# Kernel tuning notes

Measured on AMD Instinct MI355X. Metric: run time of the kernel, lower is better.

## Reference

```python
import jax, jax.numpy as jnp
import numpy as np

D_MODEL = 2048
N_HEAD = 16
HEAD_DIM = D_MODEL // N_HEAD
FF_MULT = 4
LN_EPS = 1e-5


def layer_norm(x, w, b):
    mu = jnp.mean(x, axis=-1, keepdims=True)
    var = jnp.mean(jnp.square(x - mu), axis=-1, keepdims=True)
    return (x - mu) * jax.lax.rsqrt(var + LN_EPS) * w + b


def setup_inputs() -> dict:
    key = jax.random.key(0)
    ks = jax.random.split(key, 10)
    B, S, D = 2, 2048, D_MODEL
    s = 1.0 / np.sqrt(D)
    inp = {
        "x": jax.random.normal(ks[0], (B, S, D), jnp.float32),
        "token_emb": jax.random.normal(ks[1], (B, S, D), jnp.float32),
        # torch Linear weights are (out_features, in_features)
        "Wq": jax.random.normal(ks[2], (D, D), jnp.float32) * s,
        "Wk": jax.random.normal(ks[3], (D, D), jnp.float32) * s,
        "Wv": jax.random.normal(ks[4], (D, D), jnp.float32) * s,
        "Wo": jax.random.normal(ks[5], (D, D), jnp.float32) * s,
        "W1": jax.random.normal(ks[6], (FF_MULT * D, D), jnp.float32) * s,
        "W2": jax.random.normal(ks[7], (D, FF_MULT * D), jnp.float32) * (1.0 / np.sqrt(FF_MULT * D)),
        "ln1_w": jnp.ones((D,), jnp.float32),
        "ln1_b": jnp.zeros((D,), jnp.float32),
        "ln2_w": jnp.ones((D,), jnp.float32),
        "ln2_b": jnp.zeros((D,), jnp.float32),
    }
    return inp


def reference(x, token_emb, Wq, Wk, Wv, Wo, W1, W2, ln1_w, ln1_b, ln2_w, ln2_b):
    B, S, D = x.shape
    H, Hd = N_HEAD, HEAD_DIM

    h_norm = layer_norm(x, ln1_w, ln1_b)
    # torch Linear: y = x @ W.T
    q = (h_norm @ Wq.T).reshape(B, S, H, Hd).transpose(0, 2, 1, 3)  # (B,H,S,Hd)
    k = (h_norm @ Wk.T).reshape(B, S, H, Hd).transpose(0, 2, 1, 3)
    v = (token_emb @ Wv.T).reshape(B, S, H, Hd).transpose(0, 2, 1, 3)

    scores = jnp.einsum("bhqd,bhkd->bhqk", q, k) / np.sqrt(Hd)
    causal = jnp.tril(jnp.ones((S, S), bool))  # (S,S)
    scores = jnp.where(causal, scores, -jnp.inf)
    weights = jax.nn.softmax(scores, axis=-1)

    attn = jnp.einsum("bhqk,bhkd->bhqd", weights, v)
    attn = attn.transpose(0, 2, 1, 3).reshape(B, S, D)
    attn = attn @ Wo.T
    x = x + attn

    h_ffn = layer_norm(x, ln2_w, ln2_b)
    ffn = jax.nn.gelu(h_ffn @ W1.T, approximate=False) @ W2.T
    return x + ffn
```

## Files before the change

kernel.cpp:

```cpp
#include <hip/hip_runtime.h>
#include <hip/hip_bf16.h>
#include <math.h>

#define D_MODEL 2048
#define SEQ     2048
#define BATCH   2
#define NTOK    (BATCH*SEQ)
#define NHEAD   16
#define HDIM    128
#define FF      8192

typedef float  f32x4  __attribute__((ext_vector_type(4)));
typedef __bf16 bf16x8 __attribute__((ext_vector_type(8)));

__device__ __forceinline__ unsigned short f2bfbits(float f) {
    unsigned u = __builtin_bit_cast(unsigned, f);
    return (unsigned short)((u + 0x7fffu + ((u >> 16) & 1u)) >> 16);
}
__device__ __forceinline__ __bf16 f2bf(float f) {
    unsigned short h = f2bfbits(f);
    return __builtin_bit_cast(__bf16, h);
}

__device__ __forceinline__ void gld_lds16(const void* g, void* l) {
    __builtin_amdgcn_global_load_lds(
        (const __attribute__((address_space(1))) unsigned int*)g,
        (__attribute__((address_space(3))) unsigned int*)l, 16, 0, 0);
}

__global__ __launch_bounds__(256) void cvt_all(
        const float* __restrict__ tok, const float* __restrict__ wq,
        const float* __restrict__ wk,  const float* __restrict__ wv,
        const float* __restrict__ wo,  const float* __restrict__ w1,
        const float* __restrict__ w2,
        __bf16* __restrict__ tokb, __bf16* __restrict__ wqb,
        __bf16* __restrict__ wkb,  __bf16* __restrict__ wvb,
        __bf16* __restrict__ wob,  __bf16* __restrict__ w1b,
        __bf16* __restrict__ w2b) {
    const size_t M4 = 4u * 1024 * 1024;
    size_t i = (size_t)blockIdx.x * 1024 + (size_t)threadIdx.x * 4;
    const float* src; __bf16* dst; size_t off;
    if      (i < 2*M4)  { src = tok; dst = tokb; off = i; }
    else if (i < 3*M4)  { src = wq;  dst = wqb;  off = i - 2*M4; }
    else if (i < 4*M4)  { src = wk;  dst = wkb;  off = i - 3*M4; }
    else if (i < 5*M4)  { src = wv;  dst = wvb;  off = i - 4*M4; }
    else if (i < 6*M4)  { src = wo;  dst = wob;  off = i - 5*M4; }
    else if (i < 10*M4) { src = w1;  dst = w1b;  off = i - 6*M4; }
    else                { src = w2;  dst = w2b;  off = i - 10*M4; }
    float4 v = *(const float4*)(src + off);
    ushort4 o;
    o.x = f2bfbits(v.x); o.y = f2bfbits(v.y);
    o.z = f2bfbits(v.z); o.w = f2bfbits(v.w);
    *(ushort4*)((unsigned short*)dst + off) = o;
}

__global__ __launch_bounds__(256) void add_reduce(
        const float* __restrict__ p0, const float* __restrict__ p1,
        const float* __restrict__ resid, float* __restrict__ out) {
    int i = blockIdx.x * 256 + threadIdx.x;
    float4 a = ((const float4*)p0)[i];
    float4 b = ((const float4*)p1)[i];
    float4 r = ((const float4*)resid)[i];
    float4 o;
    o.x = a.x + b.x + r.x; o.y = a.y + b.y + r.y;
    o.z = a.z + b.z + r.z; o.w = a.w + b.w + r.w;
    ((float4*)out)[i] = o;
}

__global__ __launch_bounds__(256) void ln_bf16(
        const float* __restrict__ x, const float* __restrict__ w,
        const float* __restrict__ b, __bf16* __restrict__ out) {
    const int row = blockIdx.x;
    const int tid = threadIdx.x;
    const float* xr = x + (size_t)row * D_MODEL;
    float4 v0 = *(const float4*)(xr + tid * 8);
    float4 v1 = *(const float4*)(xr + tid * 8 + 4);
    float va[8] = {v0.x, v0.y, v0.z, v0.w, v1.x, v1.y, v1.z, v1.w};
    float s = 0.f, ss = 0.f;
#pragma unroll
    for (int j = 0; j < 8; ++j) { s += va[j]; ss += va[j] * va[j]; }
#pragma unroll
    for (int m = 32; m; m >>= 1) { s += __shfl_xor(s, m, 64); ss += __shfl_xor(ss, m, 64); }
    __shared__ float red[8];
    const int wid = tid >> 6;
    if ((tid & 63) == 0) { red[wid * 2] = s; red[wid * 2 + 1] = ss; }
    __syncthreads();
    s  = red[0] + red[2] + red[4] + red[6];
    ss = red[1] + red[3] + red[5] + red[7];
    const float mu   = s * (1.0f / D_MODEL);
    const float var  = ss * (1.0f / D_MODEL) - mu * mu;
    const float rstd = rsqrtf(var + 1e-5f);
    const int c = tid * 8;
    ushort4 o0, o1;
    unsigned short ob[8];
#pragma unroll
    for (int j = 0; j < 8; ++j)
        ob[j] = f2bfbits((va[j] - mu) * rstd * w[c + j] + b[c + j]);
    o0.x = ob[0]; o0.y = ob[1]; o0.z = ob[2]; o0.w = ob[3];
    o1.x = ob[4]; o1.y = ob[5]; o1.z = ob[6]; o1.w = ob[7];
    ushort4* op = (ushort4*)(out + (size_t)row * D_MODEL + c);
    op[0] = o0; op[1] = o1;
}


template <int EPI, int MM>
__device__ __forceinline__ void gemm_epi(
        f32x4 (*acc)[4], int BMsz, int WMsz,
        int bm, int bn, int wm, int wn, int lhi, int l16,
        int M, int N, int slice,
        __bf16* __restrict__ Cb, float* __restrict__ Cf,
        const float* __restrict__ resid) {
#pragma unroll
    for (int m = 0; m < MM; ++m) {
        const int row = bm * BMsz + wm * WMsz + m * 16 + lhi * 4;
#pragma unroll
        for (int n = 0; n < 4; ++n) {
            const int col = bn * 256 + wn * 64 + n * 16 + l16;
            if (EPI == 3) {
                const int h = col >> 7, hd = col & 127;
                const size_t obase =
                    ((((size_t)(row >> 11) * NHEAD + h) * HDIM + hd) << 11) + (row & 2047);
                ushort4 o;
                o.x = f2bfbits(acc[m][n][0]); o.y = f2bfbits(acc[m][n][1]);
                o.z = f2bfbits(acc[m][n][2]); o.w = f2bfbits(acc[m][n][3]);
                *(ushort4*)((unsigned short*)Cb + obase) = o;
            } else {
#pragma unroll
                for (int r = 0; r < 4; ++r) {
                    float v = acc[m][n][r];
                    size_t off = (size_t)(row + r) * N + col;
                    if (EPI == 0) {
                        Cb[off] = f2bf(v);
                    } else if (EPI == 1) {
                        Cb[off] = f2bf(0.5f * v * (1.0f + erff(v * 0.70710678118654752f)));
                    } else if (EPI == 2) {
                        Cf[off] = v + resid[off];
                    } else {
                        Cf[(size_t)slice * M * N + off] = v;
                    }
                }
            }
        }
    }
}

template <int EPI, int SPLITK, int GEO>
__device__ __forceinline__ void gemm_core(
        const __bf16* __restrict__ A, const __bf16* __restrict__ Bm,
        __bf16* __restrict__ Cb, float* __restrict__ Cf,
        const float* __restrict__ resid, int M, int N, int K,
        int bm, int bn, int slice, char* smem) {
    const int tid = threadIdx.x;
    const int wid = tid >> 6, lane = tid & 63;
    const int l16 = lane & 15, lhi = lane >> 4;
    const int wm = wid >> 2, wn = wid & 3;
    const int tps = (K >> 6) / SPLITK;
    const int t0 = slice * tps, t1 = t0 + tps;

    auto stage128 = [&](char* dst, const __bf16* G, int kt, int rowOff) {
#pragma unroll
        for (int j = 0; j < 2; ++j) {
            int idx = j * 512 + tid;
            int r = idx >> 3;
            int Xc = (idx & 7) << 4;
            int Xs = Xc ^ ((r & 7) << 4);
            gld_lds16((const char*)(G + ((size_t)(rowOff + r) * K + kt * 64)) + Xs,
                      dst + idx * 16);
        }
    };

    if constexpr (GEO == 0) {
        const __bf16* Ag = A  + (size_t)bm * 256 * K;
        const __bf16* Bg = Bm + (size_t)bn * 256 * K;
        f32x4 acc[8][4] = {};
        bf16x8 af0[4][2], af1[4][2], bq0[2][2], bq1[2][2];
        const char *Ab_, *Bb_;
        auto ldA = [&](bf16x8 (&dst)[4][2], int qm) {
#pragma unroll
            for (int i = 0; i < 4; ++i)
#pragma unroll
                for (int ks = 0; ks < 2; ++ks) {
                    int r = wm * 128 + (qm * 4 + i) * 16 + l16;
                    int X = ks * 64 + lhi * 16;
                    dst[i][ks] = *(const bf16x8*)(Ab_ + r * 128 + (X ^ ((r & 7) << 4)));
                }
        };
        auto ldB = [&](bf16x8 (&dst)[2][2], int qn) {
#pragma unroll
            for (int j = 0; j < 2; ++j)
#pragma unroll
                for (int ks = 0; ks < 2; ++ks) {
                    int r = wn * 64 + (qn * 2 + j) * 16 + l16;
                    int X = ks * 64 + lhi * 16;
                    dst[j][ks] = *(const bf16x8*)(Bb_ + r * 128 + (X ^ ((r & 7) << 4)));
                }
        };
        auto mfmaQ = [&](bf16x8 (&a)[4][2], bf16x8 (&b)[2][2], int mo, int no) {
            __builtin_amdgcn_s_setprio(1);
#pragma unroll
            for (int i = 0; i < 4; ++i)
#pragma unroll
                for (int j = 0; j < 2; ++j)
#pragma unroll
                    for (int ks = 0; ks < 2; ++ks)
                        acc[mo + i][no + j] = __builtin_amdgcn_mfma_f32_16x16x32_bf16(
                            a[i][ks], b[j][ks], acc[mo + i][no + j], 0, 0, 0);
            __builtin_amdgcn_s_setprio(0);
        };
        auto stageT = [&](int t, int c) {
            char* base = smem + c * 65536;
            stage128(base,         Ag, t, 0);
            stage128(base + 16384, Ag, t, 128);
            stage128(base + 32768, Bg, t, 0);
            stage128(base + 49152, Bg, t, 128);
        };

        stageT(t0, 0);
        asm volatile("s_waitcnt vmcnt(0)" ::: "memory");
        __builtin_amdgcn_s_barrier();

        for (int t = t0; t < t1; ++t) {
            const int cur = (t - t0) & 1;
            Ab_ = smem + cur * 65536;
            Bb_ = Ab_ + 32768;
            const bool pf = (t + 1 < t1);
            if (pf) stageT(t + 1, cur ^ 1);
            ldA(af0, 0); ldB(bq0, 0);
            __builtin_amdgcn_s_barrier();
            asm volatile("s_waitcnt lgkmcnt(0)" ::: "memory");
            __builtin_amdgcn_sched_barrier(0);
            mfmaQ(af0, bq0, 0, 0);
            __builtin_amdgcn_s_barrier();
            ldB(bq1, 1);
            __builtin_amdgcn_s_barrier();
            asm volatile("s_waitcnt lgkmcnt(0)" ::: "memory");
            __builtin_amdgcn_sched_barrier(0);
            mfmaQ(af0, bq1, 0, 2);
            __builtin_amdgcn_s_barrier();
            ldA(af1, 1);
            __builtin_amdgcn_s_barrier();
            asm volatile("s_waitcnt lgkmcnt(0)" ::: "memory");
            __builtin_amdgcn_sched_barrier(0);
            mfmaQ(af1, bq0, 4, 0);
            __builtin_amdgcn_s_barrier();
            mfmaQ(af1, bq1, 4, 2);
            if (pf) asm volatile("s_waitcnt vmcnt(0)" ::: "memory");
            __builtin_amdgcn_s_barrier();
        }
        gemm_epi<EPI, 8>(acc, 256, 128, bm, bn, wm, wn, lhi, l16,
                         M, N, slice, Cb, Cf, resid);
    } else {
        const __bf16* Ag = A  + (size_t)bm * 128 * K;
        const __bf16* Bg = Bm + (size_t)bn * 256 * K;
        f32x4 acc[4][4] = {};
        auto stageT = [&](int t, int c) {
            char* base = smem + c * 49152;
            stage128(base,         Ag, t, 0);
            stage128(base + 16384, Bg, t, 0);
            stage128(base + 32768, Bg, t, 128);
        };
        stageT(t0, 0);
        if (t0 + 1 < t1) {
            stageT(t0 + 1, 1);
            asm volatile("s_waitcnt vmcnt(6)" ::: "memory");
        } else {
            asm volatile("s_waitcnt vmcnt(0)" ::: "memory");
        }
        __builtin_amdgcn_s_barrier();

        for (int t = t0; t < t1; ++t) {
            const int c = (t - t0) % 3;
            if (t + 2 < t1) stageT(t + 2, (c + 2) % 3);
            const char* Ab_ = smem + c * 49152;
            const char* Bb_ = Ab_ + 16384;
            bf16x8 af[4][2], bq[4][2];
#pragma unroll
            for (int i = 0; i < 4; ++i)
#pragma unroll
                for (int ks = 0; ks < 2; ++ks) {
                    int r = wm * 64 + i * 16 + l16;
                    int X = ks * 64 + lhi * 16;
                    af[i][ks] = *(const bf16x8*)(Ab_ + r * 128 + (X ^ ((r & 7) << 4)));
                }
#pragma unroll
            for (int j = 0; j < 4; ++j)
#pragma unroll
                for (int ks = 0; ks < 2; ++ks) {
                    int r = wn * 64 + j * 16 + l16;
                    int X = ks * 64 + lhi * 16;
                    bq[j][ks] = *(const bf16x8*)(Bb_ + r * 128 + (X ^ ((r & 7) << 4)));
                }
            asm volatile("s_waitcnt lgkmcnt(0)" ::: "memory");
            __builtin_amdgcn_sched_barrier(0);
            __builtin_amdgcn_s_setprio(1);
#pragma unroll
            for (int i = 0; i < 4; ++i)
#pragma unroll
                for (int j = 0; j < 4; ++j)
#pragma unroll
                    for (int ks = 0; ks < 2; ++ks)
                        acc[i][j] = __builtin_amdgcn_mfma_f32_16x16x32_bf16(
                            af[i][ks], bq[j][ks], acc[i][j], 0, 0, 0);
            __builtin_amdgcn_s_setprio(0);
            if (t + 2 < t1) {
                asm volatile("s_waitcnt vmcnt(6)" ::: "memory");
                __builtin_amdgcn_s_barrier();
            } else if (t + 1 < t1) {
                asm volatile("s_waitcnt vmcnt(0)" ::: "memory");
                __builtin_amdgcn_s_barrier();
            }
        }
        gemm_epi<EPI, 4>(acc, 128, 64, bm, bn, wm, wn, lhi, l16,
                         M, N, slice, Cb, Cf, resid);
    }
}

template <int EPI, int SPLITK, int GEO, int MAP>
__global__ __launch_bounds__(512, 2) void gemm_k(
        const __bf16* __restrict__ A, const __bf16* __restrict__ Bm,
        __bf16* __restrict__ Cb, float* __restrict__ Cf,
        const float* __restrict__ resid, int M, int N, int K) {
    __shared__ __align__(16) char smem[GEO ? 147456 : 131072];
    int bm, bn, slice = 0;
    if (MAP == 0) {
        int id = blockIdx.x;
        const int cpx = gridDim.x >> 3;
        id = (id & 7) * cpx + (id >> 3);
        const int nbn = N >> 8;
        if (SPLITK == 2) {
            const int nblk = (M >> (GEO ? 7 : 8)) * nbn;
            slice = id / nblk;
            id -= slice * nblk;
        }
        bm = id / nbn; bn = id % nbn;
    } else if (MAP == 1) {
        const int x = blockIdx.x & 7, j = blockIdx.x >> 3;
        bn = (x << 2) | (j & 3); bm = j >> 2;
    } else {
        const int x = blockIdx.x & 7, j = blockIdx.x >> 3;
        bm = (x << 2) | (j & 3); bn = j >> 2;
    }
    gemm_core<EPI, SPLITK, GEO>(A, Bm, Cb, Cf, resid, M, N, K, bm, bn, slice, smem);
}

__global__ __launch_bounds__(512, 2) void gemm_qkv(
        const __bf16* __restrict__ hn, const __bf16* __restrict__ wqk,
        __bf16* __restrict__ QKb, const __bf16* __restrict__ tokb,
        const __bf16* __restrict__ wv, __bf16* __restrict__ Vtg) {
    __shared__ __align__(16) char smem[147456];
    const int x = blockIdx.x & 7, j = blockIdx.x >> 3;
    if (j < 32) {
        const int bm = ((x >> 1) << 2) | (j & 3);
        const int bn = ((x & 1) << 3) | (j >> 2);
        gemm_core<0, 1, 0>(hn, wqk, QKb, nullptr, nullptr,
                           NTOK, 2 * D_MODEL, D_MODEL, bm, bn, 0, smem);
    } else {
        const int jv = j - 32;
        const int bm = ((x >> 1) << 3) | (jv & 7);
        const int bn = ((x & 1) << 2) | (jv >> 3);
        gemm_core<3, 1, 1>(tokb, wv, Vtg, nullptr, nullptr,
                           NTOK, D_MODEL, D_MODEL, bm, bn, 0, smem);
    }
}

#define LDQK 4096
__global__ __launch_bounds__(512) void attn_causal(
        const __bf16* __restrict__ Q, const __bf16* __restrict__ K,
        const __bf16* __restrict__ Vt, __bf16* __restrict__ O) {
    const int qt = gridDim.x - 1 - blockIdx.x;
    const int h = blockIdx.y, bb = blockIdx.z;
    const int tid = threadIdx.x, wid = tid >> 6, lane = tid & 63;
    const int l16 = lane & 15, lhi = lane >> 4;
    __shared__ __align__(16) __bf16 Ks[2][64 * 128];
    __shared__ __align__(16) __bf16 Vs[128 * 64];
    __shared__ __align__(16) __bf16 Pl[8][16 * 72];

    const size_t qkbase = ((size_t)bb * SEQ) * LDQK + (size_t)h * HDIM;
    const size_t obase  = ((size_t)bb * SEQ) * D_MODEL + (size_t)h * HDIM;
    const size_t vtbase = (((size_t)bb * NHEAD + h) * HDIM) << 11;
    const int q0 = qt * 128 + wid * 16;

    bf16x8 qf[4];
#pragma unroll
    for (int ks = 0; ks < 4; ++ks)
        qf[ks] = *(const bf16x8*)(Q + qkbase + (size_t)(q0 + l16) * LDQK + ks * 32 + lhi * 8);

    auto stageK = [&](int kt, int buf) {
#pragma unroll
        for (int j = 0; j < 2; ++j) {
            int idx = j * 512 + tid;
            int row = idx >> 4, c8 = idx & 15;
            int c8s = c8 ^ (row & 7);
            gld_lds16(K + qkbase + (size_t)(kt * 64 + row) * LDQK + c8s * 8,
                      &Ks[buf][0] + idx * 8);
        }
    };
    auto stageV = [&](int kt) {
#pragma unroll
        for (int j = 0; j < 2; ++j) {
            int idx = j * 512 + tid;
            int row = idx >> 3, c8 = idx & 7;
            int c8s = c8 ^ (row & 7);
            gld_lds16(Vt + vtbase + (size_t)row * SEQ + kt * 64 + c8s * 8, Vs + idx * 8);
        }
    };

    f32x4 accO[8] = {};
    float m_run[4], l_run[4];
#pragma unroll
    for (int r = 0; r < 4; ++r) { m_run[r] = -1e30f; l_run[r] = 0.f; }

    const float scale2 = 0.08838834764831845f * 1.4426950408889634f;
    const int NKT = (qt + 1) * 2;

    stageK(0, 0);
    asm volatile("s_waitcnt vmcnt(0)" ::: "memory");
    __builtin_amdgcn_s_barrier();
    __builtin_amdgcn_sched_barrier(0);

    for (int kt = 0; kt < NKT; ++kt) {
        const int cb = kt & 1;
        const bool pf = (kt + 1 < NKT);
        stageV(kt);
        if (pf) stageK(kt + 1, cb ^ 1);

        f32x4 s[4] = {};
        __builtin_amdgcn_s_setprio(1);
#pragma unroll
        for (int nb = 0; nb < 4; ++nb) {
            const int tok = nb * 16 + l16;
#pragma unroll
            for (int ks = 0; ks < 4; ++ks) {
                int co = (ks * 64 + lhi * 16) ^ ((tok & 7) << 4);
                bf16x8 kf = *(const bf16x8*)((const char*)&Ks[cb][0] + tok * 256 + co);
                s[nb] = __builtin_amdgcn_mfma_f32_16x16x32_bf16(qf[ks], kf, s[nb], 0, 0, 0);
            }
        }
        __builtin_amdgcn_s_setprio(0);

        if (((kt + 1) << 6) > q0) {
#pragma unroll
            for (int nb = 0; nb < 4; ++nb)
#pragma unroll
                for (int r = 0; r < 4; ++r) {
                    float sv = s[nb][r] * scale2;
                    if ((kt * 64 + nb * 16 + l16) > (q0 + lhi * 4 + r)) sv = -1e30f;
                    s[nb][r] = sv;
                }
        } else {
#pragma unroll
            for (int nb = 0; nb < 4; ++nb)
#pragma unroll
                for (int r = 0; r < 4; ++r) s[nb][r] *= scale2;
        }

        float alpha[4];
#pragma unroll
        for (int r = 0; r < 4; ++r) {
            float mx = fmaxf(fmaxf(s[0][r], s[1][r]), fmaxf(s[2][r], s[3][r]));
#pragma unroll
            for (int m = 8; m; m >>= 1) mx = fmaxf(mx, __shfl_xor(mx, m, 64));
            float mnew = fmaxf(m_run[r], mx);
            alpha[r] = exp2f(m_run[r] - mnew);
            float rs = 0.f;
#pragma unroll
            for (int nb = 0; nb < 4; ++nb) {
                float p = exp2f(s[nb][r] - mnew);
                s[nb][r] = p;
                rs += p;
            }
#pragma unroll
            for (int m = 8; m; m >>= 1) rs += __shfl_xor(rs, m, 64);
            l_run[r] = l_run[r] * alpha[r] + rs;
            m_run[r] = mnew;
        }
#pragma unroll
        for (int d8 = 0; d8 < 8; ++d8)
#pragma unroll
            for (int r = 0; r < 4; ++r) accO[d8][r] *= alpha[r];
#pragma unroll
        for (int nb = 0; nb < 4; ++nb)
#pragma unroll
            for (int r = 0; r < 4; ++r)
                Pl[wid][(lhi * 4 + r) * 72 + nb * 16 + l16] = f2bf(s[nb][r]);

        if (pf) asm volatile("s_waitcnt vmcnt(2)" ::: "memory");
        else    asm volatile("s_waitcnt vmcnt(0)" ::: "memory");
        __builtin_amdgcn_s_barrier();
        __builtin_amdgcn_sched_barrier(0);

        __builtin_amdgcn_s_setprio(1);
#pragma unroll
        for (int ks2 = 0; ks2 < 2; ++ks2) {
            bf16x8 pa = *(const bf16x8*)(&Pl[wid][l16 * 72 + ks2 * 32 + lhi * 8]);
#pragma unroll
            for (int d8 = 0; d8 < 8; ++d8) {
                const int d = d8 * 16 + l16;
                const int co = ((ks2 * 4 + lhi) ^ (d & 7)) << 4;
                bf16x8 vf = *(const bf16x8*)((const char*)Vs + d * 128 + co);
                accO[d8] = __builtin_amdgcn_mfma_f32_16x16x32_bf16(pa, vf, accO[d8], 0, 0, 0);
            }
        }
        __builtin_amdgcn_s_setprio(0);

        asm volatile("s_waitcnt vmcnt(0)" ::: "memory");
        __builtin_amdgcn_s_barrier();
        __builtin_amdgcn_sched_barrier(0);
    }

#pragma unroll
    for (int d8 = 0; d8 < 8; ++d8)
#pragma unroll
        for (int r = 0; r < 4; ++r) {
            float o = accO[d8][r] / l_run[r];
            O[obase + (size_t)(q0 + lhi * 4 + r) * D_MODEL + d8 * 16 + l16] = f2bf(o);
        }
}

extern "C" void kernel_launch(void* const* d_in, const int* in_sizes, int n_in,
                              void* d_out, int out_size, void* d_ws, size_t ws_size,
                              hipStream_t stream) {
    const float* x    = (const float*)d_in[0];
    const float* tok  = (const float*)d_in[1];
    const float* Wq   = (const float*)d_in[2];
    const float* Wk   = (const float*)d_in[3];
    const float* Wv   = (const float*)d_in[4];
    const float* Wo   = (const float*)d_in[5];
    const float* W1   = (const float*)d_in[6];
    const float* W2   = (const float*)d_in[7];
    const float* ln1w = (const float*)d_in[8];
    const float* ln1b = (const float*)d_in[9];
    const float* ln2w = (const float*)d_in[10];
    const float* ln2b = (const float*)d_in[11];
    float* out = (float*)d_out;

    char* ws = (char*)d_ws;
    size_t off = 0;
    auto alloc = [&](size_t bytes) { void* p = ws + off; off += bytes; return p; };
    __bf16* tokb  = (__bf16*)alloc((size_t)NTOK * D_MODEL * 2);
    __bf16* hnorm = (__bf16*)alloc((size_t)NTOK * D_MODEL * 2);
    __bf16* wqb   = (__bf16*)alloc((size_t)D_MODEL * D_MODEL * 2);
    __bf16* wkb   = (__bf16*)alloc((size_t)D_MODEL * D_MODEL * 2);
    __bf16* wvb   = (__bf16*)alloc((size_t)D_MODEL * D_MODEL * 2);
    __bf16* wob   = (__bf16*)alloc((size_t)D_MODEL * D_MODEL * 2);
    __bf16* w1b   = (__bf16*)alloc((size_t)FF * D_MODEL * 2);
    __bf16* w2b   = (__bf16*)alloc((size_t)D_MODEL * FF * 2);
    __bf16* QKb   = (__bf16*)alloc((size_t)NTOK * 2 * D_MODEL * 2);
    __bf16* Vtg   = (__bf16*)alloc((size_t)NTOK * D_MODEL * 2);
    __bf16* Ab    = (__bf16*)alloc((size_t)NTOK * D_MODEL * 2);
    float*  x2    = (float*)alloc((size_t)NTOK * D_MODEL * 4);
    __bf16* gb    = QKb;
    float*  p0    = (float*)(ws);
    float*  p1    = p0 + (size_t)NTOK * D_MODEL;

    cvt_all<<<56 * 1024, 256, 0, stream>>>(tok, Wq, Wk, Wv, Wo, W1, W2,
                                           tokb, wqb, wkb, wvb, wob, w1b, w2b);

    ln_bf16<<<NTOK, 256, 0, stream>>>(x, ln1w, ln1b, hnorm);

    gemm_qkv<<<512, 512, 0, stream>>>(hnorm, wqb, QKb, tokb, wvb, Vtg);

    attn_causal<<<dim3(SEQ / 128, NHEAD, BATCH), 512, 0, stream>>>(QKb, QKb + D_MODEL, Vtg, Ab);

    gemm_k<2, 1, 1, 2><<<256, 512, 0, stream>>>(Ab, wob, nullptr, x2, x,
                                                NTOK, D_MODEL, D_MODEL);

    ln_bf16<<<NTOK, 256, 0, stream>>>(x2, ln2w, ln2b, hnorm);

    gemm_k<1, 1, 0, 1><<<512, 512, 0, stream>>>(hnorm, w1b, gb, nullptr, nullptr,
                                                NTOK, FF, D_MODEL);
    gemm_k<4, 2, 0, 0><<<256, 512, 0, stream>>>(gb, w2b, nullptr, p0, nullptr,
                                                NTOK, D_MODEL, FF);
    add_reduce<<<(NTOK * D_MODEL) / 1024, 256, 0, stream>>>(p0, p1, x2, out);
}
```

Baseline: 647.7 us.

## Interleave per-half A/B prefetch into MFMA phases of the 256x256 GEMM

The large-tile GEMM main loop is unrolled by two tiles. Global-to-LDS staging of the next tile's A and B halves is now spread across the four MFMA sub-phases, instead of issuing the whole next tile up front and draining with vmcnt(0) at the end of each iteration. B is prefetched two tiles ahead and waits use partial vmcnt(4), to keep memory traffic overlapped with compute and shorten stalls. The new loop assumes the tile range starts on an even tile and has an even length. Other edits only introduce macros for barriers and waitcnt.

```diff
diff --git a/kernel.cpp b/kernel.cpp
--- a/kernel.cpp
+++ b/kernel.cpp
@@ -27,6 +27,11 @@
         (const __attribute__((address_space(1))) unsigned int*)g,
         (__attribute__((address_space(3))) unsigned int*)l, 16, 0, 0);
 }
+
+#define BAR()      __builtin_amdgcn_s_barrier()
+#define LGKM0()    asm volatile("s_waitcnt lgkmcnt(0)" ::: "memory")
+#define VMCNT(N)   asm volatile("s_waitcnt vmcnt(" #N ")" ::: "memory")
+#define SCHEDB()   __builtin_amdgcn_sched_barrier(0)
 
 __global__ __launch_bounds__(256) void cvt_all(
         const float* __restrict__ tok, const float* __restrict__ wq,
@@ -207,45 +212,63 @@
                             a[i][ks], b[j][ks], acc[mo + i][no + j], 0, 0, 0);
             __builtin_amdgcn_s_setprio(0);
         };
-        auto stageT = [&](int t, int c) {
-            char* base = smem + c * 65536;
-            stage128(base,         Ag, t, 0);
-            stage128(base + 16384, Ag, t, 128);
-            stage128(base + 32768, Bg, t, 0);
-            stage128(base + 49152, Bg, t, 128);
+        auto stA = [&](int t, int half) {
+            stage128(smem + ((t & 1) ? 65536 : 0) + half * 16384, Ag, t, half * 128);
         };
-
-        stageT(t0, 0);
-        asm volatile("s_waitcnt vmcnt(0)" ::: "memory");
-        __builtin_amdgcn_s_barrier();
-
-        for (int t = t0; t < t1; ++t) {
-            const int cur = (t - t0) & 1;
-            Ab_ = smem + cur * 65536;
-            Bb_ = Ab_ + 32768;
-            const bool pf = (t + 1 < t1);
-            if (pf) stageT(t + 1, cur ^ 1);
+        auto stB = [&](int t, int half) {
+            stage128(smem + ((t & 1) ? 98304 : 32768) + half * 16384, Bg, t, half * 128);
+        };
+
+        stA(t0, 0); stA(t0, 1);
+        stB(t0, 0); stB(t0, 1);
+        stB(t0 + 1, 0); stB(t0 + 1, 1);
+        VMCNT(4);
+        BAR();
+
+        for (int ta = t0; ta < t1; ta += 2) {
+            const int tb = ta + 1;
+            const bool pf = (ta + 2 < t1);
+            Ab_ = smem; Bb_ = smem + 32768;
             ldA(af0, 0); ldB(bq0, 0);
-            __builtin_amdgcn_s_barrier();
-            asm volatile("s_waitcnt lgkmcnt(0)" ::: "memory");
-            __builtin_amdgcn_sched_barrier(0);
+            stA(tb, 0);
+            BAR(); LGKM0(); SCHEDB();
             mfmaQ(af0, bq0, 0, 0);
-            __builtin_amdgcn_s_barrier();
+            BAR();
             ldB(bq1, 1);
-            __builtin_amdgcn_s_barrier();
-            asm volatile("s_waitcnt lgkmcnt(0)" ::: "memory");
-            __builtin_amdgcn_sched_barrier(0);
+            stA(tb, 1);
+            BAR(); LGKM0(); SCHEDB();
             mfmaQ(af0, bq1, 0, 2);
-            __builtin_amdgcn_s_barrier();
+            BAR();
             ldA(af1, 1);
-            __builtin_amdgcn_s_barrier();
-            asm volatile("s_waitcnt lgkmcnt(0)" ::: "memory");
-            __builtin_amdgcn_sched_barrier(0);
+            if (pf) stB(ta + 2, 0);
+            BAR(); LGKM0(); SCHEDB();
             mfmaQ(af1, bq0, 4, 0);
-            __builtin_amdgcn_s_barrier();
+            BAR();
+            if (pf) stB(ta + 2, 1);
+            BAR(); SCHEDB();
             mfmaQ(af1, bq1, 4, 2);
-            if (pf) asm volatile("s_waitcnt vmcnt(0)" ::: "memory");
-            __builtin_amdgcn_s_barrier();
+            if (pf) { VMCNT(4); } else { VMCNT(0); }
+            BAR();
+            Ab_ = smem + 65536; Bb_ = smem + 98304;
+            ldA(af0, 0); ldB(bq0, 0);
+            if (pf) stA(ta + 2, 0);
+            BAR(); LGKM0(); SCHEDB();
+            mfmaQ(af0, bq0, 0, 0);
+            BAR();
+            ldB(bq1, 1);
+            if (pf) stA(ta + 2, 1);
+            BAR(); LGKM0(); SCHEDB();
+            mfmaQ(af0, bq1, 0, 2);
+            BAR();
+            ldA(af1, 1);
+            if (pf) stB(ta + 3, 0);
+            BAR(); LGKM0(); SCHEDB();
+            mfmaQ(af1, bq0, 4, 0);
+            BAR();
+            if (pf) stB(ta + 3, 1);
+            BAR(); SCHEDB();
+            mfmaQ(af1, bq1, 4, 2);
+            if (pf) { VMCNT(4); BAR(); }
         }
         gemm_epi<EPI, 8>(acc, 256, 128, bm, bn, wm, wn, lhi, l16,
                          M, N, slice, Cb, Cf, resid);
@@ -262,11 +285,11 @@
         stageT(t0, 0);
         if (t0 + 1 < t1) {
             stageT(t0 + 1, 1);
-            asm volatile("s_waitcnt vmcnt(6)" ::: "memory");
+            VMCNT(6);
         } else {
-            asm volatile("s_waitcnt vmcnt(0)" ::: "memory");
-        }
-        __builtin_amdgcn_s_barrier();
+            VMCNT(0);
+        }
+        BAR();
 
         for (int t = t0; t < t1; ++t) {
             const int c = (t - t0) % 3;
@@ -290,8 +313,7 @@
                     int X = ks * 64 + lhi * 16;
                     bq[j][ks] = *(const bf16x8*)(Bb_ + r * 128 + (X ^ ((r & 7) << 4)));
                 }
-            asm volatile("s_waitcnt lgkmcnt(0)" ::: "memory");
-            __builtin_amdgcn_sched_barrier(0);
+            LGKM0(); SCHEDB();
             __builtin_amdgcn_s_setprio(1);
 #pragma unroll
             for (int i = 0; i < 4; ++i)
@@ -303,11 +325,11 @@
                             af[i][ks], bq[j][ks], acc[i][j], 0, 0, 0);
             __builtin_amdgcn_s_setprio(0);
             if (t + 2 < t1) {
-                asm volatile("s_waitcnt vmcnt(6)" ::: "memory");
-                __builtin_amdgcn_s_barrier();
+                VMCNT(6);
+                BAR();
             } else if (t + 1 < t1) {
-                asm volatile("s_waitcnt vmcnt(0)" ::: "memory");
-                __builtin_amdgcn_s_barrier();
+                VMCNT(0);
+                BAR();
             }
         }
         gemm_epi<EPI, 4>(acc, 128, 64, bm, bn, wm, wn, lhi, l16,
@@ -414,9 +436,9 @@
     const int NKT = (qt + 1) * 2;
 
     stageK(0, 0);
-    asm volatile("s_waitcnt vmcnt(0)" ::: "memory");
-    __builtin_amdgcn_s_barrier();
-    __builtin_amdgcn_sched_barrier(0);
+    VMCNT(0);
+    BAR();
+    SCHEDB();
 
     for (int kt = 0; kt < NKT; ++kt) {
         const int cb = kt & 1;
@@ -484,10 +506,9 @@
             for (int r = 0; r < 4; ++r)
                 Pl[wid][(lhi * 4 + r) * 72 + nb * 16 + l16] = f2bf(s[nb][r]);
 
-        if (pf) asm volatile("s_waitcnt vmcnt(2)" ::: "memory");
-        else    asm volatile("s_waitcnt vmcnt(0)" ::: "memory");
-        __builtin_amdgcn_s_barrier();
-        __builtin_amdgcn_sched_barrier(0);
+        if (pf) { VMCNT(2); } else { VMCNT(0); }
+        BAR();
+        SCHEDB();
 
         __builtin_amdgcn_s_setprio(1);
 #pragma unroll
@@ -503,9 +524,9 @@
         }
         __builtin_amdgcn_s_setprio(0);
 
-        asm volatile("s_waitcnt vmcnt(0)" ::: "memory");
-        __builtin_amdgcn_s_barrier();
-        __builtin_amdgcn_sched_barrier(0);
+        VMCNT(0);
+        BAR();
+        SCHEDB();
     }
 
 #pragma unroll
```

Result: no change. 653.4 us (+0.9%).
